# Kernel tuning notes

Hardware: AMD Instinct MI355X
Metric: run time of the kernel (lower is better)

Reference implementation:

```python
import jax, jax.numpy as jnp
import numpy as np

D_MODEL, HID, N_NODES, NODE_DIM = 128, 256, 17, 32

def _gelu(x):
    return jax.nn.gelu(x, approximate=False)  # torch nn.GELU default (erf)

def setup_inputs() -> dict:
    key = jax.random.key(0)
    ks = jax.random.split(key, 12)
    B, W = 16, 4096
    x = jax.random.normal(ks[0], (B, W, D_MODEL), dtype=jnp.float32)
    # node_proj: Linear(128,256) -> GELU -> Linear(256, 17*32)
    W1 = jax.random.normal(ks[1], (D_MODEL, HID), dtype=jnp.float32) / np.sqrt(D_MODEL)
    b1 = jnp.zeros((HID,), jnp.float32)
    W2 = jax.random.normal(ks[2], (HID, N_NODES * NODE_DIM), dtype=jnp.float32) / np.sqrt(HID)
    b2 = jnp.zeros((N_NODES * NODE_DIM,), jnp.float32)
    # GAT1
    adj1 = jnp.eye(N_NODES, dtype=jnp.float32) * 5.0 + jax.random.normal(ks[3], (N_NODES, N_NODES), jnp.float32) * 0.05
    Wg1 = jax.random.normal(ks[4], (NODE_DIM, NODE_DIM), dtype=jnp.float32) / np.sqrt(NODE_DIM)
    bg1 = jnp.zeros((NODE_DIM,), jnp.float32)
    # GAT2
    adj2 = jnp.eye(N_NODES, dtype=jnp.float32) * 5.0 + jax.random.normal(ks[5], (N_NODES, N_NODES), jnp.float32) * 0.05
    Wg2 = jax.random.normal(ks[6], (NODE_DIM, NODE_DIM), dtype=jnp.float32) / np.sqrt(NODE_DIM)
    bg2 = jnp.zeros((NODE_DIM,), jnp.float32)
    # coord_proj: Linear(32, 2)
    Wc = jax.random.normal(ks[7], (NODE_DIM, 2), dtype=jnp.float32) / np.sqrt(NODE_DIM)
    bc = jnp.zeros((2,), jnp.float32)
    return {"x": x, "W1": W1, "b1": b1, "W2": W2, "b2": b2,
            "adj1": adj1, "Wg1": Wg1, "bg1": bg1,
            "adj2": adj2, "Wg2": Wg2, "bg2": bg2,
            "Wc": Wc, "bc": bc}

def _gat(nodes, adj_logits, Wg, bg):
    # nodes: [B, W, N, F]
    adj = jax.nn.softmax(adj_logits, axis=-1)          # [N, N]
    mixed = jnp.einsum('ij,bwjf->bwif', adj, nodes)    # graph conv over 17 joints
    return _gelu(mixed @ Wg + bg) + nodes              # linear-GELU + residual

def reference(x, W1, b1, W2, b2, adj1, Wg1, bg1, adj2, Wg2, bg2, Wc, bc):
    B, W, _ = x.shape
    h = _gelu(x @ W1 + b1)                 # [B, W, 256] (dropout inactive at eval)
    nodes = (h @ W2 + b2).reshape(B, W, N_NODES, NODE_DIM)
    out = _gat(nodes, adj1, Wg1, bg1)
    out = _gat(out, adj2, Wg2, bg2)
    return out @ Wc + bc                   # [B, W, 17, 2]
```

## Files before the change

### kernel.cpp

```cpp
#include <hip/hip_runtime.h>
#include <hip/hip_bf16.h>

using bf16 = __hip_bfloat16;
typedef __bf16 bf16x4v __attribute__((ext_vector_type(4)));
typedef __bf16 bf16x8 __attribute__((ext_vector_type(8)));
typedef float f32x4 __attribute__((ext_vector_type(4)));

#define MT 32
#define SX 136
#define SH 264
#define SJ 20
#define TFS 640
#define NTF_ELEMS 20480
#define MS_BASE 20496
#define SMS 36
#define MSW 1440
#define S_ELEMS 32304

__device__ __forceinline__ float bf2f(bf16 v) { return __bfloat162float(v); }

__device__ __forceinline__ float gelu_f(float x) {
    float u  = 0.7978845608f * x * (1.0f + 0.044715f * x * x);
    float au = fabsf(u);
    float e  = __expf(-2.0f * au);
    float t  = (1.0f - e) / (1.0f + e);
    t = (u < 0.0f) ? -t : t;
    return 0.5f * x * (1.0f + t);
}

__device__ __forceinline__ bf16x8 ld8(const bf16* p) {
    return *reinterpret_cast<const bf16x8*>(p);
}
__device__ __forceinline__ bf16x8 ld8u(const bf16* p) {
    bf16x4v lo = *reinterpret_cast<const bf16x4v*>(p);
    bf16x4v hi = *reinterpret_cast<const bf16x4v*>(p + 4);
    return __builtin_shufflevector(lo, hi, 0, 1, 2, 3, 4, 5, 6, 7);
}
__device__ __forceinline__ f32x4 mfma16(bf16x8 a, bf16x8 b, f32x4 c) {
    return __builtin_amdgcn_mfma_f32_16x16x32_bf16(a, b, c, 0, 0, 0);
}

__global__ void prep_kernel(const float* __restrict__ W1, const float* __restrict__ W2,
                            const float* __restrict__ Wg1, const float* __restrict__ Wg2,
                            const float* __restrict__ adj1, const float* __restrict__ adj2,
                            bf16* __restrict__ w1t, bf16* __restrict__ w2t,
                            bf16* __restrict__ wg1t, bf16* __restrict__ wg2t,
                            float* __restrict__ A1f, float* __restrict__ A2f) {
    int idx = blockIdx.x * 256 + threadIdx.x;
    if (idx < 32768) {
        int r = idx >> 8, c = idx & 255;
        w1t[c * 128 + r] = __float2bfloat16(W1[idx]);
    } else if (idx < 172032) {
        int j = idx - 32768;
        int r = j / 544, c = j % 544;
        w2t[c * 256 + r] = __float2bfloat16(W2[j]);
    } else if (idx < 173056) {
        int j = idx - 172032;
        wg1t[(j & 31) * 32 + (j >> 5)] = __float2bfloat16(Wg1[j]);
    } else if (idx < 174080) {
        int j = idx - 173056;
        wg2t[(j & 31) * 32 + (j >> 5)] = __float2bfloat16(Wg2[j]);
    }
    if (blockIdx.x == 0) {
        int t = threadIdx.x;
        if (t < 17 || (t >= 32 && t < 49)) {
            const float* adj = (t < 17) ? adj1 : adj2;
            float*       A   = (t < 17) ? A1f  : A2f;
            int row = (t < 17) ? t : (t - 32);
            float v[17]; float mx = -1e30f;
            for (int j = 0; j < 17; ++j) { v[j] = adj[row * 17 + j]; mx = fmaxf(mx, v[j]); }
            float s = 0.0f;
            for (int j = 0; j < 17; ++j) { v[j] = __expf(v[j] - mx); s += v[j]; }
            float inv = 1.0f / s;
            for (int j = 0; j < 17; ++j) A[row * 17 + j] = v[j] * inv;
        }
    }
}

__global__ __launch_bounds__(512, 4)
void gat_main(const float* __restrict__ x,
              const float* __restrict__ b1, const float* __restrict__ b2,
              const float* __restrict__ bg1, const float* __restrict__ bg2,
              const bf16* __restrict__ w1t, const bf16* __restrict__ w2t,
              const bf16* __restrict__ wg1t, const bf16* __restrict__ wg2t,
              const float* __restrict__ A1, const float* __restrict__ A2,
              const float* __restrict__ Wc, const float* __restrict__ bc,
              float* __restrict__ out) {
    __shared__ alignas(16) bf16 S[S_ELEMS];
    bf16* xs = S;
    bf16* hs = S + 4352;

    const int tid  = threadIdx.x;
    const int w    = tid >> 6;
    const int lane = tid & 63;
    const int l    = lane & 15;
    const int q    = lane >> 4;
    const int t0   = blockIdx.x * MT;

    for (int c = tid; c < 1024; c += 512) {
        int row = c >> 5, c4 = c & 31;
        const float4 v = *reinterpret_cast<const float4*>(x + (size_t)(t0 + row) * 128 + c4 * 4);
        bf16 tmp[4] = { __float2bfloat16(v.x), __float2bfloat16(v.y),
                        __float2bfloat16(v.z), __float2bfloat16(v.w) };
        *reinterpret_cast<ushort4*>(xs + row * SX + c4 * 4) =
            *reinterpret_cast<const ushort4*>(tmp);
    }
    __syncthreads();

    for (int nt = w * 2; nt < w * 2 + 2; ++nt) {
        int n = nt * 16 + l;
        bf16x8 bfr[4];
        const bf16* wp = w1t + n * 128 + q * 8;
#pragma unroll
        for (int kf = 0; kf < 4; ++kf) bfr[kf] = ld8(wp + kf * 32);
        float bias = b1[n];
#pragma unroll
        for (int mt = 0; mt < 2; ++mt) {
            f32x4 acc = {0.f, 0.f, 0.f, 0.f};
            const bf16* ap = xs + (mt * 16 + l) * SX + q * 8;
#pragma unroll
            for (int kf = 0; kf < 4; ++kf)
                acc = mfma16(ld8(ap + kf * 32), bfr[kf], acc);
            int trow = mt * 16 + q * 4;
#pragma unroll
            for (int r = 0; r < 4; ++r)
                hs[(trow + r) * SH + n] = __float2bfloat16(gelu_f(acc[r] + bias));
        }
    }
    __syncthreads();

    {
        bf16x8 af[2][8];
#pragma unroll
        for (int mt = 0; mt < 2; ++mt)
#pragma unroll
            for (int kf = 0; kf < 8; ++kf)
                af[mt][kf] = ld8(hs + (mt * 16 + l) * SH + kf * 32 + q * 8);
        __syncthreads();

        for (int z = tid; z < 3072; z += 512) {
            int row = z / 3, k = z - row * 3;
            S[row * SJ + 17 + k] = __float2bfloat16(0.f);
        }
        if (tid < 16) S[NTF_ELEMS + tid] = __float2bfloat16(0.f);

        for (int nt = w; nt < 34; nt += 8) {
            int n = nt * 16 + l;
            float bias = b2[n];
            int i = n >> 5, f = n & 31;
            f32x4 a0 = {0.f, 0.f, 0.f, 0.f}, a1 = {0.f, 0.f, 0.f, 0.f};
            const bf16* wp = w2t + n * 256 + q * 8;
#pragma unroll
            for (int kf = 0; kf < 8; ++kf) {
                bf16x8 bfr = ld8(wp + kf * 32);
                a0 = mfma16(af[0][kf], bfr, a0);
                a1 = mfma16(af[1][kf], bfr, a1);
            }
#pragma unroll
            for (int mt = 0; mt < 2; ++mt) {
                const f32x4 acc = mt ? a1 : a0;
#pragma unroll
                for (int r = 0; r < 4; ++r) {
                    int t = mt * 16 + q * 4 + r;
                    S[t * TFS + f * SJ + i] = __float2bfloat16(acc[r] + bias);
                }
            }
        }
    }
    __syncthreads();

    bf16* ms_w = S + MS_BASE + w * MSW;

    for (int g = 0; g < 2; ++g) {
        const float* A  = g ? A2 : A1;
        const bf16* wgt = g ? wg2t : wg1t;
        const float* bg = g ? bg2 : bg1;

        bf16x8 mixB[2];
#pragma unroll
        for (int nt = 0; nt < 2; ++nt) {
            int i = nt * 16 + l;
            bf16 tmp[8];
#pragma unroll
            for (int e = 0; e < 8; ++e) {
                int j = q * 8 + e;
                float v = (i < 17 && j < 17) ? A[i * 17 + j] : 0.0f;
                tmp[e] = __float2bfloat16(v);
            }
            mixB[nt] = *reinterpret_cast<bf16x8*>(tmp);
        }
        bf16x8 wfr[2];
#pragma unroll
        for (int nt = 0; nt < 2; ++nt) wfr[nt] = ld8(wgt + (nt * 16 + l) * 32 + q * 8);
        float bgf[2] = { bg[l], bg[16 + l] };

        for (int c = 0; c < 2; ++c) {
#pragma unroll
            for (int mt2 = 0; mt2 < 4; ++mt2) {
                int R = w * 128 + c * 64 + mt2 * 16 + l;
                bf16x8 afr = ld8u(S + R * SJ + q * 8);
                int rr0 = mt2 * 16 + q * 4;
                int f0  = rr0 & 31;
                int tl  = rr0 >> 5;
#pragma unroll
                for (int nt = 0; nt < 2; ++nt) {
                    f32x4 acc = {0.f, 0.f, 0.f, 0.f};
                    acc = mfma16(afr, mixB[nt], acc);
                    int i = nt * 16 + l;
                    if (i < 17) {
                        union { ushort4 u; bf16 b[4]; } pk;
#pragma unroll
                        for (int r = 0; r < 4; ++r) pk.b[r] = __float2bfloat16(acc[r]);
                        *reinterpret_cast<ushort4*>(ms_w + (i * 2 + tl) * SMS + f0) = pk.u;
                    }
                }
            }

#pragma unroll
            for (int mt = 0; mt < 3; ++mt) {
                bf16x8 afr = ld8u(ms_w + (mt * 16 + l) * SMS + q * 8);
#pragma unroll
                for (int nt = 0; nt < 2; ++nt) {
                    f32x4 acc = {0.f, 0.f, 0.f, 0.f};
                    acc = mfma16(afr, wfr[nt], acc);
                    int fp = nt * 16 + l;
#pragma unroll
                    for (int r = 0; r < 4; ++r) {
                        int rr = mt * 16 + q * 4 + r;
                        int i  = rr >> 1;
                        int tl = rr & 1;
                        if (i < 17) {
                            int off = (w * 4 + c * 2 + tl) * TFS + fp * SJ + i;
                            float v = gelu_f(acc[r] + bgf[nt]) + bf2f(S[off]);
                            S[off]  = __float2bfloat16(v);
                        }
                    }
                }
            }
        }
    }

    for (int s = lane; s < 68; s += 64) {
        int tl = s / 17, i = s - tl * 17;
        int t  = w * 4 + tl;
        const bf16* gp = S + t * TFS + i;
        float o0 = bc[0], o1 = bc[1];
#pragma unroll
        for (int f = 0; f < 32; ++f) {
            float v = bf2f(gp[f * SJ]);
            o0 = fmaf(v, Wc[f * 2 + 0], o0);
            o1 = fmaf(v, Wc[f * 2 + 1], o1);
        }
        float2 pr = { o0, o1 };
        reinterpret_cast<float2*>(out)[(size_t)(t0 + t) * 17 + i] = pr;
    }
}

extern "C" void kernel_launch(void* const* d_in, const int* in_sizes, int n_in,
                              void* d_out, int out_size, void* d_ws, size_t ws_size,
                              hipStream_t stream) {
    const float* x    = (const float*)d_in[0];
    const float* W1   = (const float*)d_in[1];
    const float* b1   = (const float*)d_in[2];
    const float* W2   = (const float*)d_in[3];
    const float* b2   = (const float*)d_in[4];
    const float* adj1 = (const float*)d_in[5];
    const float* Wg1  = (const float*)d_in[6];
    const float* bg1  = (const float*)d_in[7];
    const float* adj2 = (const float*)d_in[8];
    const float* Wg2  = (const float*)d_in[9];
    const float* bg2  = (const float*)d_in[10];
    const float* Wc   = (const float*)d_in[11];
    const float* bc   = (const float*)d_in[12];

    char* ws = (char*)d_ws;
    bf16*  w1t  = (bf16*)(ws + 0);
    bf16*  w2t  = (bf16*)(ws + 65536);
    bf16*  wg1t = (bf16*)(ws + 344064);
    bf16*  wg2t = (bf16*)(ws + 346112);
    float* A1f  = (float*)(ws + 348160);
    float* A2f  = (float*)(ws + 349376);

    prep_kernel<<<680, 256, 0, stream>>>(W1, W2, Wg1, Wg2, adj1, adj2,
                                         w1t, w2t, wg1t, wg2t, A1f, A2f);

    const int tokens = 16 * 4096;
    gat_main<<<tokens / MT, 512, 0, stream>>>(x, b1, b2, bg1, bg2,
                                              w1t, w2t, wg1t, wg2t,
                                              A1f, A2f, Wc, bc, (float*)d_out);
}
```

Before: 249.8 us.

## Process one timestep per GAT chunk with vectorized residual writes and cheaper GELU

Measured after the change: 236.0 us. 5.5% less time.

```diff
diff --git a/kernel.cpp b/kernel.cpp
--- a/kernel.cpp
+++ b/kernel.cpp
@@ -14,18 +14,19 @@
 #define NTF_ELEMS 20480
 #define MS_BASE 20496
 #define SMS 36
-#define MSW 1440
-#define S_ELEMS 32304
+#define MSW 612
+#define S_ELEMS 25936
 
 __device__ __forceinline__ float bf2f(bf16 v) { return __bfloat162float(v); }
 
 __device__ __forceinline__ float gelu_f(float x) {
-    float u  = 0.7978845608f * x * (1.0f + 0.044715f * x * x);
+    float u  = x * fmaf(0.035677408f * x, x, 0.7978845608f);
     float au = fabsf(u);
     float e  = __expf(-2.0f * au);
-    float t  = (1.0f - e) / (1.0f + e);
+    float t  = (1.0f - e) * __builtin_amdgcn_rcpf(1.0f + e);
     t = (u < 0.0f) ? -t : t;
-    return 0.5f * x * (1.0f + t);
+    float hx = 0.5f * x;
+    return fmaf(hx, t, hx);
 }
 
 __device__ __forceinline__ bf16x8 ld8(const bf16* p) {
@@ -194,14 +195,14 @@
         for (int nt = 0; nt < 2; ++nt) wfr[nt] = ld8(wgt + (nt * 16 + l) * 32 + q * 8);
         float bgf[2] = { bg[l], bg[16 + l] };
 
-        for (int c = 0; c < 2; ++c) {
-#pragma unroll
-            for (int mt2 = 0; mt2 < 4; ++mt2) {
-                int R = w * 128 + c * 64 + mt2 * 16 + l;
+        for (int c = 0; c < 4; ++c) {
+            const int T = w * 4 + c;
+
+#pragma unroll
+            for (int mt2 = 0; mt2 < 2; ++mt2) {
+                int R = T * 32 + mt2 * 16 + l;
                 bf16x8 afr = ld8u(S + R * SJ + q * 8);
-                int rr0 = mt2 * 16 + q * 4;
-                int f0  = rr0 & 31;
-                int tl  = rr0 >> 5;
+                int f0 = mt2 * 16 + q * 4;
 #pragma unroll
                 for (int nt = 0; nt < 2; ++nt) {
                     f32x4 acc = {0.f, 0.f, 0.f, 0.f};
@@ -211,29 +212,31 @@
                         union { ushort4 u; bf16 b[4]; } pk;
 #pragma unroll
                         for (int r = 0; r < 4; ++r) pk.b[r] = __float2bfloat16(acc[r]);
-                        *reinterpret_cast<ushort4*>(ms_w + (i * 2 + tl) * SMS + f0) = pk.u;
+                        *reinterpret_cast<ushort4*>(ms_w + i * SMS + f0) = pk.u;
                     }
                 }
             }
 
 #pragma unroll
-            for (int mt = 0; mt < 3; ++mt) {
+            for (int mt = 0; mt < 2; ++mt) {
                 bf16x8 afr = ld8u(ms_w + (mt * 16 + l) * SMS + q * 8);
+                int i0 = mt * 16 + q * 4;
 #pragma unroll
                 for (int nt = 0; nt < 2; ++nt) {
                     f32x4 acc = {0.f, 0.f, 0.f, 0.f};
                     acc = mfma16(afr, wfr[nt], acc);
                     int fp = nt * 16 + l;
-#pragma unroll
-                    for (int r = 0; r < 4; ++r) {
-                        int rr = mt * 16 + q * 4 + r;
-                        int i  = rr >> 1;
-                        int tl = rr & 1;
-                        if (i < 17) {
-                            int off = (w * 4 + c * 2 + tl) * TFS + fp * SJ + i;
-                            float v = gelu_f(acc[r] + bgf[nt]) + bf2f(S[off]);
-                            S[off]  = __float2bfloat16(v);
+                    if (i0 < 17) {
+                        bf16* p = S + T * TFS + fp * SJ + i0;
+                        union { ushort4 u; bf16 b[4]; } old, nw;
+                        old.u = *reinterpret_cast<const ushort4*>(p);
+#pragma unroll
+                        for (int r = 0; r < 4; ++r) {
+                            float v = gelu_f(acc[r] + bgf[nt]) + bf2f(old.b[r]);
+                            if (i0 + r > 16) v = 0.0f;
+                            nw.b[r] = __float2bfloat16(v);
                         }
+                        *reinterpret_cast<ushort4*>(p) = nw.u;
                     }
                 }
             }
```
